# Kernel tuning notes

Measured on AMD Instinct MI355X. Metric: run time of the kernel, lower is better.

Reference implementation:

```python
import jax, jax.numpy as jnp
import numpy as np

POOL, D_MODEL, D_FF, M_DIM = 512, 1024, 4096, 64
B, S, K = 2, 2048, 8


def setup_inputs() -> dict:
    key = jax.random.key(0)
    ks = jax.random.split(key, 8)
    x = jax.random.normal(ks[0], (B, S, D_MODEL), dtype=jnp.float32)
    selected_indices = jax.random.randint(ks[1], (B, S, K), 0, POOL, dtype=jnp.int32)
    pattern_weights = jax.random.normal(ks[2], (B, S, K), dtype=jnp.float32)
    base_patterns = 0.02 * jax.random.normal(ks[3], (POOL, D_FF), dtype=jnp.float32)
    # nn.Linear(d_model, pool_size*mod_dim): weight [P*M, d_model], xavier-uniform
    lim_cm = float(np.sqrt(6.0 / (D_MODEL + POOL * M_DIM)))
    cm_w = jax.random.uniform(ks[4], (POOL * M_DIM, D_MODEL), jnp.float32, -lim_cm, lim_cm)
    cm_b = jnp.zeros((POOL * M_DIM,), jnp.float32)
    adj_proj = 0.01 * jax.random.normal(ks[5], (M_DIM, D_FF), dtype=jnp.float32)
    lim_w2 = float(np.sqrt(6.0 / (D_FF + D_MODEL)))
    w2_w = jax.random.uniform(ks[6], (D_MODEL, D_FF), jnp.float32, -lim_w2, lim_w2)
    w2_b = jnp.zeros((D_MODEL,), jnp.float32)
    return {"x": x, "selected_indices": selected_indices, "pattern_weights": pattern_weights,
            "base_patterns": base_patterns, "cm_w": cm_w, "cm_b": cm_b,
            "adj_proj": adj_proj, "w2_w": w2_w, "w2_b": w2_b}


def reference(x, selected_indices, pattern_weights, base_patterns, cm_w, cm_b, adj_proj, w2_w, w2_b):
    b, s, k = selected_indices.shape
    # gather base firing patterns for selected neurons: [b,s,k,d_ff]
    bp = base_patterns[selected_indices]
    # dense context modulation then gather (matches original module): [b,s,P,M]
    mod = (jnp.einsum('bsd,nd->bsn', x, cm_w) + cm_b).reshape(b, s, POOL, M_DIM)
    sel_mod = jnp.take_along_axis(mod, selected_indices[..., None], axis=2)  # [b,s,k,M]
    adjustments = jnp.einsum('bskm,mf->bskf', sel_mod, adj_proj)
    adjusted = bp + adjustments  # [b,s,k,d_ff]
    w = jax.nn.softmax(pattern_weights, axis=-1)
    combined = jnp.einsum('bsk,bskf->bsf', w, adjusted)  # [b,s,d_ff]
    activated = jax.nn.gelu(combined, approximate=False)  # torch default gelu = exact erf
    return jnp.einsum('bsf,df->bsd', activated, w2_w) + w2_b
```

## Files before the change

### kernel.cpp

```cpp
#include <hip/hip_runtime.h>
#include <math.h>

#define T_    4096
#define K_    8
#define POOL_ 512
#define DM_   1024
#define DFF_  4096
#define MD_   64
#define KC_   576
#define NCAP  256

typedef __bf16 bf16x8 __attribute__((ext_vector_type(8)));
typedef __bf16 bf16x4 __attribute__((ext_vector_type(4)));
typedef float  f32x4  __attribute__((ext_vector_type(4)));

typedef __attribute__((address_space(1))) const void g_void;
typedef __attribute__((address_space(3))) void s_void;

__device__ __forceinline__ void async_ld16(const void* g, void* s) {
    __builtin_amdgcn_global_load_lds((g_void*)g, (s_void*)s, 16, 0, 0);
}
__device__ __forceinline__ float gelu_exact(float g) {
    return 0.5f * g * (1.f + erff(g * 0.70710678118654752f));
}
__device__ __forceinline__ bf16x4 cvt4(float4 v) {
    bf16x4 o;
    o[0] = (__bf16)v.x; o[1] = (__bf16)v.y; o[2] = (__bf16)v.z; o[3] = (__bf16)v.w;
    return o;
}

__global__ __launch_bounds__(256) void k_hist(const int* __restrict__ sel,
                                              int* __restrict__ counts) {
    int i = blockIdx.x * 256 + threadIdx.x;
    if (i < T_ * K_) atomicAdd(&counts[sel[i]], 1);
}

__global__ __launch_bounds__(512) void k_scan(const int* __restrict__ counts,
                                              int* __restrict__ offsets,
                                              int* __restrict__ cursor) {
    __shared__ int s[512];
    const int t = threadIdx.x;
    const int c = counts[t];
    s[t] = c;
    __syncthreads();
    for (int d = 1; d < 512; d <<= 1) {
        int v = (t >= d) ? s[t - d] : 0;
        __syncthreads();
        s[t] += v;
        __syncthreads();
    }
    offsets[t] = s[t] - c;
    cursor[t]  = s[t] - c;
    if (t == 511) offsets[512] = s[511];
}

__global__ __launch_bounds__(256) void k_scatter(const int* __restrict__ sel,
                                                 int* __restrict__ cursor,
                                                 int* __restrict__ bucket,
                                                 int* __restrict__ rank) {
    int i = blockIdx.x * 256 + threadIdx.x;
    if (i < T_ * K_) {
        int p = sel[i];
        int pos = atomicAdd(&cursor[p], 1);
        bucket[pos] = i;
        rank[i] = pos;
    }
}

__global__ __launch_bounds__(256) void k_cvt(const float* __restrict__ src,
                                             __bf16* __restrict__ dst, int n16) {
    int i = blockIdx.x * 256 + threadIdx.x;
    if (i >= n16) return;
    const float4* s = (const float4*)src + (long)i * 4;
    float4 a = s[0], b = s[1], c = s[2], d = s[3];
    bf16x8 o0, o1;
    o0[0]=(__bf16)a.x; o0[1]=(__bf16)a.y; o0[2]=(__bf16)a.z; o0[3]=(__bf16)a.w;
    o0[4]=(__bf16)b.x; o0[5]=(__bf16)b.y; o0[6]=(__bf16)b.z; o0[7]=(__bf16)b.w;
    o1[0]=(__bf16)c.x; o1[1]=(__bf16)c.y; o1[2]=(__bf16)c.z; o1[3]=(__bf16)c.w;
    o1[4]=(__bf16)d.x; o1[5]=(__bf16)d.y; o1[6]=(__bf16)d.z; o1[7]=(__bf16)d.w;
    bf16x8* dp = (bf16x8*)dst + (long)i * 2;
    dp[0] = o0; dp[1] = o1;
}

__global__ __launch_bounds__(256) void k_selmod(
    const __bf16* __restrict__ xb, const float* __restrict__ cm_w,
    const int* __restrict__ bucket, const int* __restrict__ offsets,
    float* __restrict__ Y)
{
    const int p   = blockIdx.x;
    const int ms  = blockIdx.y;
    const int tid = threadIdx.x;
    __shared__ int list[NCAP];
    __shared__ __align__(16) __bf16 Wl[16][1032];
    __shared__ __align__(16) __bf16 Xl[64][72];

    const int off = offsets[p];
    const int n   = min(offsets[p + 1] - off, NCAP);
    if (n == 0) return;
    for (int i = tid; i < n; i += 256) list[i] = bucket[off + i] >> 3;

    {
        const int wr = tid >> 4;
        const int wl = tid & 15;
        const float* wsrc = cm_w + (long)(p * 64 + ms * 16 + wr) * DM_;
        #pragma unroll
        for (int j = 0; j < 16; ++j) {
            float4 v = *(const float4*)(wsrc + j * 64 + wl * 4);
            *(bf16x4*)&Wl[wr][j * 64 + wl * 4] = cvt4(v);
        }
    }
    __syncthreads();

    const int wave = tid >> 6, lane = tid & 63, quad = lane >> 4, l15 = lane & 15;
    const int srow = tid >> 3;
    const int part = tid & 7;

    for (int base = 0; base < n; base += 64) {
        f32x4 acc = {};
        int li0 = base + srow;      if (li0 >= n) li0 = n - 1;
        int li1 = base + srow + 32; if (li1 >= n) li1 = n - 1;
        const __bf16* x0 = xb + (long)list[li0] * DM_ + part * 8;
        const __bf16* x1 = xb + (long)list[li1] * DM_ + part * 8;

        for (int kc = 0; kc < DM_; kc += 64) {
            *(bf16x8*)&Xl[srow     ][part * 8] = *(const bf16x8*)(x0 + kc);
            *(bf16x8*)&Xl[srow + 32][part * 8] = *(const bf16x8*)(x1 + kc);
            __syncthreads();
            #pragma unroll
            for (int ks = 0; ks < 2; ++ks) {
                const int ko = ks * 32 + quad * 8;
                bf16x8 bfr = *(const bf16x8*)&Wl[l15][kc + ko];
                bf16x8 afr = *(const bf16x8*)&Xl[wave * 16 + l15][ko];
                acc = __builtin_amdgcn_mfma_f32_16x16x32_bf16(afr, bfr, acc, 0, 0, 0);
            }
            __syncthreads();
        }
        #pragma unroll
        for (int r = 0; r < 4; ++r) {
            int prow = base + wave * 16 + quad * 4 + r;
            if (prow < n)
                Y[(long)(off + prow) * MD_ + ms * 16 + l15] = acc[r];
        }
    }
}

__global__ __launch_bounds__(256) void k_wdense(
    const float* __restrict__ Y, const int* __restrict__ sel,
    const int* __restrict__ rank, const float* __restrict__ pw,
    const float* __restrict__ cm_b, __bf16* __restrict__ Wd)
{
    const int tid = threadIdx.x;
    const int tt = tid >> 6, m = tid & 63;
    const int t = blockIdx.x * 4 + tt;
    __shared__ float w_s[4][8];
    __shared__ int   sidx[4][8];
    __shared__ int   rnk[4][8];
    __shared__ __align__(16) __bf16 row[4][KC_];

    if (m < 8) {
        w_s[tt][m]  = pw[t * 8 + m];
        sidx[tt][m] = sel[t * 8 + m];
        rnk[tt][m]  = rank[t * 8 + m];
    }
    __syncthreads();
    if (m == 0) {
        float mx = w_s[tt][0];
        #pragma unroll
        for (int k = 1; k < 8; ++k) mx = fmaxf(mx, w_s[tt][k]);
        float sum = 0.f;
        #pragma unroll
        for (int k = 0; k < 8; ++k) { float e = expf(w_s[tt][k] - mx); w_s[tt][k] = e; sum += e; }
        float inv = 1.f / sum;
        #pragma unroll
        for (int k = 0; k < 8; ++k) w_s[tt][k] *= inv;
    }
    __syncthreads();
    *(uint4*)&row[tt][m * 8] = make_uint4(0, 0, 0, 0);
    {
        float a = 0.f;
        #pragma unroll
        for (int k = 0; k < 8; ++k) {
            float y = cm_b[sidx[tt][k] * 64 + m] + Y[(long)rnk[tt][k] * MD_ + m];
            a += w_s[tt][k] * y;
        }
        row[tt][512 + m] = (__bf16)a;
    }
    __syncthreads();
    if (m == 0) {
        #pragma unroll
        for (int k = 0; k < 8; ++k) {
            int c = sidx[tt][k];
            row[tt][c] = (__bf16)((float)row[tt][c] + w_s[tt][k]);
        }
    }
    __syncthreads();
    const uint4* src = (const uint4*)&row[0][0];
    uint4* dst = (uint4*)(Wd + (long)blockIdx.x * 4 * KC_);
    for (int e = tid; e < 4 * KC_ * 2 / 16; e += 256) dst[e] = src[e];
}

__global__ __launch_bounds__(256) void k_buildP(
    const float* __restrict__ bp, const float* __restrict__ adj,
    __bf16* __restrict__ P)
{
    __shared__ __bf16 tile[64][72];
    const int tid = threadIdx.x;
    const int bx = blockIdx.x, f0 = blockIdx.y * 64;
    const float* src = (bx < 8) ? (bp + (long)bx * 64 * DFF_) : adj;
    for (int e = tid; e < 4096; e += 256) {
        int f = e & 63, c = e >> 6;
        tile[c][f] = (__bf16)src[(long)c * DFF_ + f0 + f];
    }
    __syncthreads();
    const int c0 = bx * 64;
    for (int e = tid; e < 4096; e += 256) {
        int c = e & 63, f = e >> 6;
        P[(long)(f0 + f) * KC_ + c0 + c] = tile[c][f];
    }
}

__global__ __launch_bounds__(256) void k_actgemm(
    const __bf16* __restrict__ A, const __bf16* __restrict__ Bw,
    __bf16* __restrict__ act)
{
    __shared__ __align__(16) __bf16 sA[128 * 32];
    __shared__ __align__(16) __bf16 sB[128 * 32];
    const int tid  = threadIdx.x;
    const int tm   = blockIdx.y * 128, tn = blockIdx.x * 128;
    const int wave = tid >> 6, lane = tid & 63, quad = lane >> 4, l15 = lane & 15;
    const int wm   = (wave >> 1) * 64, wn = (wave & 1) * 64;

    f32x4 acc[4][4] = {};

    const int e    = tid * 8;
    const int srow = e >> 5;
    const int scol = e & 31;
    const __bf16* agp0 = A  + ((long)(tm + srow)      * KC_ + scol);
    const __bf16* agp1 = A  + ((long)(tm + 64 + srow) * KC_ + scol);
    const __bf16* bgp0 = Bw + ((long)(tn + srow)      * KC_ + scol);
    const __bf16* bgp1 = Bw + ((long)(tn + 64 + srow) * KC_ + scol);
    void* sa0 = (void*)(sA + e);
    void* sa1 = (void*)(sA + 2048 + e);
    void* sb0 = (void*)(sB + e);
    void* sb1 = (void*)(sB + 2048 + e);

    for (int kk = 0; kk < KC_; kk += 32) {
        async_ld16(agp0 + kk, sa0);
        async_ld16(agp1 + kk, sa1);
        async_ld16(bgp0 + kk, sb0);
        async_ld16(bgp1 + kk, sb1);
        __syncthreads();
        bf16x8 af[4], bf[4];
        #pragma unroll
        for (int i = 0; i < 4; ++i)
            af[i] = *(const bf16x8*)(sA + (wm + i * 16 + l15) * 32 + quad * 8);
        #pragma unroll
        for (int j = 0; j < 4; ++j)
            bf[j] = *(const bf16x8*)(sB + (wn + j * 16 + l15) * 32 + quad * 8);
        #pragma unroll
        for (int i = 0; i < 4; ++i)
            #pragma unroll
            for (int j = 0; j < 4; ++j)
                acc[i][j] = __builtin_amdgcn_mfma_f32_16x16x32_bf16(af[i], bf[j], acc[i][j], 0, 0, 0);
        __syncthreads();
    }

    #pragma unroll
    for (int j = 0; j < 4; ++j) {
        const int col = tn + wn + j * 16 + l15;
        #pragma unroll
        for (int i = 0; i < 4; ++i) {
            const int row = tm + wm + i * 16 + quad * 4;
            #pragma unroll
            for (int r = 0; r < 4; ++r)
                act[(long)(row + r) * DFF_ + col] = (__bf16)gelu_exact(acc[i][j][r]);
        }
    }
}

__global__ __launch_bounds__(256) void k_outgemm(
    const __bf16* __restrict__ A, const __bf16* __restrict__ Bw,
    const float* __restrict__ bias, float* __restrict__ out)
{
    __shared__ __align__(16) __bf16 sA[128 * 128];
    __shared__ __align__(16) __bf16 sB[128 * 128];
    const int tid  = threadIdx.x;
    const int tm   = blockIdx.y * 128, tn = blockIdx.x * 128;
    const int wave = tid >> 6, lane = tid & 63, quad = lane >> 4, l15 = lane & 15;
    const int wm   = (wave >> 1) * 64, wn = (wave & 1) * 64;

    f32x4 acc[4][4] = {};

    const int e  = tid * 8;
    const int r0 = e >> 5;
    const int cc = e & 31;

    for (int kk = 0; kk < DFF_; kk += 128) {
        #pragma unroll
        for (int s = 0; s < 4; ++s) {
            #pragma unroll
            for (int q = 0; q < 2; ++q) {
                async_ld16(A  + (long)(tm + q * 64 + r0) * DFF_ + kk + s * 32 + cc,
                           (void*)(sA + s * 4096 + q * 2048 + e));
                async_ld16(Bw + (long)(tn + q * 64 + r0) * DFF_ + kk + s * 32 + cc,
                           (void*)(sB + s * 4096 + q * 2048 + e));
            }
        }
        __syncthreads();
        #pragma unroll
        for (int s = 0; s < 4; ++s) {
            bf16x8 af[4], bf[4];
            #pragma unroll
            for (int i = 0; i < 4; ++i)
                af[i] = *(const bf16x8*)(sA + s * 4096 + (wm + i * 16 + l15) * 32 + quad * 8);
            #pragma unroll
            for (int j = 0; j < 4; ++j)
                bf[j] = *(const bf16x8*)(sB + s * 4096 + (wn + j * 16 + l15) * 32 + quad * 8);
            #pragma unroll
            for (int i = 0; i < 4; ++i)
                #pragma unroll
                for (int j = 0; j < 4; ++j)
                    acc[i][j] = __builtin_amdgcn_mfma_f32_16x16x32_bf16(af[i], bf[j], acc[i][j], 0, 0, 0);
        }
        __syncthreads();
    }

    #pragma unroll
    for (int j = 0; j < 4; ++j) {
        const int col = tn + wn + j * 16 + l15;
        const float bj = bias[col];
        #pragma unroll
        for (int i = 0; i < 4; ++i) {
            const int row = tm + wm + i * 16 + quad * 4;
            #pragma unroll
            for (int r = 0; r < 4; ++r)
                out[(long)(row + r) * 1024 + col] = acc[i][j][r] + bj;
        }
    }
}

extern "C" void kernel_launch(void* const* d_in, const int* in_sizes, int n_in,
                              void* d_out, int out_size, void* d_ws, size_t ws_size,
                              hipStream_t stream) {
    const float* x    = (const float*)d_in[0];
    const int*   sel  = (const int*)  d_in[1];
    const float* pw   = (const float*)d_in[2];
    const float* bp   = (const float*)d_in[3];
    const float* cm_w = (const float*)d_in[4];
    const float* cm_b = (const float*)d_in[5];
    const float* adj  = (const float*)d_in[6];
    const float* w2   = (const float*)d_in[7];
    const float* w2b  = (const float*)d_in[8];
    float* out = (float*)d_out;

    char* ws = (char*)d_ws;
    __bf16* x_bf = (__bf16*)ws;
    __bf16* act  = (__bf16*)ws;
    __bf16* P    = (__bf16*)(ws + (size_t)32 * 1024 * 1024);
    __bf16* w2bf = (__bf16*)(ws + (size_t)37 * 1024 * 1024);
    char*  bins  = ws + (size_t)45 * 1024 * 1024;
    int* bucket  = (int*)bins;
    int* rank    = (int*)(bins + 131072);
    int* counts  = (int*)(bins + 262144);
    int* cursor  = (int*)(bins + 264192);
    int* offsets = (int*)(bins + 266240);

    float*  Y  = (float*)d_out;
    __bf16* Wd = (__bf16*)((char*)d_out + (size_t)8 * 1024 * 1024);

    hipMemsetAsync(counts, 0, 4096, stream);
    k_hist   <<<128, 256, 0, stream>>>(sel, counts);
    k_scan   <<<1,   512, 0, stream>>>(counts, offsets, cursor);
    k_scatter<<<128, 256, 0, stream>>>(sel, cursor, bucket, rank);
    k_cvt    <<<1024, 256, 0, stream>>>(x, x_bf, T_ * DM_ / 16);
    k_selmod <<<dim3(POOL_, 4), 256, 0, stream>>>(x_bf, cm_w, bucket, offsets, Y);
    k_wdense <<<T_ / 4, 256, 0, stream>>>(Y, sel, rank, pw, cm_b, Wd);
    k_buildP <<<dim3(9, 64), 256, 0, stream>>>(bp, adj, P);
    k_cvt    <<<1024, 256, 0, stream>>>(w2, w2bf, DM_ * DFF_ / 16);
    k_actgemm<<<dim3(DFF_ / 128, T_ / 128), 256, 0, stream>>>(Wd, P, act);
    k_outgemm<<<dim3(DM_ / 128, T_ / 128), 256, 0, stream>>>(act, w2bf, w2b, out);
}
```

Before: 415.2 us.

## Drop LDS staging in selmod; stream fragments directly from global per wave

Result: slower. 444.7 us (+7.1%).

```diff
diff --git a/kernel.cpp b/kernel.cpp
--- a/kernel.cpp
+++ b/kernel.cpp
@@ -8,7 +8,6 @@
 #define DFF_  4096
 #define MD_   64
 #define KC_   576
-#define NCAP  256
 
 typedef __bf16 bf16x8 __attribute__((ext_vector_type(8)));
 typedef __bf16 bf16x4 __attribute__((ext_vector_type(4)));
@@ -26,6 +25,12 @@
 __device__ __forceinline__ bf16x4 cvt4(float4 v) {
     bf16x4 o;
     o[0] = (__bf16)v.x; o[1] = (__bf16)v.y; o[2] = (__bf16)v.z; o[3] = (__bf16)v.w;
+    return o;
+}
+__device__ __forceinline__ bf16x8 cvt8(float4 a, float4 b) {
+    bf16x8 o;
+    o[0] = (__bf16)a.x; o[1] = (__bf16)a.y; o[2] = (__bf16)a.z; o[3] = (__bf16)a.w;
+    o[4] = (__bf16)b.x; o[5] = (__bf16)b.y; o[6] = (__bf16)b.z; o[7] = (__bf16)b.w;
     return o;
 }
 
@@ -73,11 +78,7 @@
     if (i >= n16) return;
     const float4* s = (const float4*)src + (long)i * 4;
     float4 a = s[0], b = s[1], c = s[2], d = s[3];
-    bf16x8 o0, o1;
-    o0[0]=(__bf16)a.x; o0[1]=(__bf16)a.y; o0[2]=(__bf16)a.z; o0[3]=(__bf16)a.w;
-    o0[4]=(__bf16)b.x; o0[5]=(__bf16)b.y; o0[6]=(__bf16)b.z; o0[7]=(__bf16)b.w;
-    o1[0]=(__bf16)c.x; o1[1]=(__bf16)c.y; o1[2]=(__bf16)c.z; o1[3]=(__bf16)c.w;
-    o1[4]=(__bf16)d.x; o1[5]=(__bf16)d.y; o1[6]=(__bf16)d.z; o1[7]=(__bf16)d.w;
+    bf16x8 o0 = cvt8(a, b), o1 = cvt8(c, d);
     bf16x8* dp = (bf16x8*)dst + (long)i * 2;
     dp[0] = o0; dp[1] = o1;
 }
@@ -89,55 +90,34 @@
 {
     const int p   = blockIdx.x;
     const int ms  = blockIdx.y;
-    const int tid = threadIdx.x;
-    __shared__ int list[NCAP];
-    __shared__ __align__(16) __bf16 Wl[16][1032];
-    __shared__ __align__(16) __bf16 Xl[64][72];
-
     const int off = offsets[p];
-    const int n   = min(offsets[p + 1] - off, NCAP);
+    const int n   = offsets[p + 1] - off;
     if (n == 0) return;
-    for (int i = tid; i < n; i += 256) list[i] = bucket[off + i] >> 3;
-
-    {
-        const int wr = tid >> 4;
-        const int wl = tid & 15;
-        const float* wsrc = cm_w + (long)(p * 64 + ms * 16 + wr) * DM_;
-        #pragma unroll
-        for (int j = 0; j < 16; ++j) {
-            float4 v = *(const float4*)(wsrc + j * 64 + wl * 4);
-            *(bf16x4*)&Wl[wr][j * 64 + wl * 4] = cvt4(v);
-        }
-    }
-    __syncthreads();
-
-    const int wave = tid >> 6, lane = tid & 63, quad = lane >> 4, l15 = lane & 15;
-    const int srow = tid >> 3;
-    const int part = tid & 7;
-
-    for (int base = 0; base < n; base += 64) {
+
+    const int wave = threadIdx.x >> 6, lane = threadIdx.x & 63;
+    const int quad = lane >> 4, l15 = lane & 15;
+
+    const float* wrow = cm_w + (long)(p * 64 + ms * 16 + l15) * DM_ + quad * 8;
+
+    const int nch = (n + 15) >> 4;
+    for (int c = wave; c < nch; c += 4) {
+        const int base = c * 16;
+        int row = base + l15; if (row >= n) row = n - 1;
+        const int tok = bucket[off + row] >> 3;
+        const __bf16* xrow = xb + (long)tok * DM_ + quad * 8;
+
         f32x4 acc = {};
-        int li0 = base + srow;      if (li0 >= n) li0 = n - 1;
-        int li1 = base + srow + 32; if (li1 >= n) li1 = n - 1;
-        const __bf16* x0 = xb + (long)list[li0] * DM_ + part * 8;
-        const __bf16* x1 = xb + (long)list[li1] * DM_ + part * 8;
-
-        for (int kc = 0; kc < DM_; kc += 64) {
-            *(bf16x8*)&Xl[srow     ][part * 8] = *(const bf16x8*)(x0 + kc);
-            *(bf16x8*)&Xl[srow + 32][part * 8] = *(const bf16x8*)(x1 + kc);
-            __syncthreads();
-            #pragma unroll
-            for (int ks = 0; ks < 2; ++ks) {
-                const int ko = ks * 32 + quad * 8;
-                bf16x8 bfr = *(const bf16x8*)&Wl[l15][kc + ko];
-                bf16x8 afr = *(const bf16x8*)&Xl[wave * 16 + l15][ko];
-                acc = __builtin_amdgcn_mfma_f32_16x16x32_bf16(afr, bfr, acc, 0, 0, 0);
-            }
-            __syncthreads();
+        #pragma unroll 4
+        for (int kc = 0; kc < DM_; kc += 32) {
+            bf16x8 afr = *(const bf16x8*)(xrow + kc);
+            float4 w0  = *(const float4*)(wrow + kc);
+            float4 w1  = *(const float4*)(wrow + kc + 4);
+            bf16x8 bfr = cvt8(w0, w1);
+            acc = __builtin_amdgcn_mfma_f32_16x16x32_bf16(afr, bfr, acc, 0, 0, 0);
         }
         #pragma unroll
         for (int r = 0; r < 4; ++r) {
-            int prow = base + wave * 16 + quad * 4 + r;
+            int prow = base + quad * 4 + r;
             if (prow < n)
                 Y[(long)(off + prow) * MD_ + ms * 16 + l15] = acc[r];
         }
```
